# Optimization experiments

Measured on AMD Instinct MI355X. Metric: run time of the kernel, lower is better.

The kernel has to match this reference:

```python
import jax, jax.numpy as jnp
import numpy as np

N_EMBD = 768
N_EXPERTS = 8
TOP_K = 2
D_FF = 4 * N_EMBD


def setup_inputs() -> dict:
    key = jax.random.key(0)
    k1, k2, k3, k4 = jax.random.split(key, 4)
    x = jax.random.normal(k1, (2, 2048, N_EMBD), dtype=jnp.float32)
    gate_w = jax.random.normal(k2, (N_EMBD, N_EXPERTS), dtype=jnp.float32) * (1.0 / np.sqrt(N_EMBD))
    w_fc = jax.random.normal(k3, (N_EXPERTS, N_EMBD, D_FF), dtype=jnp.float32) * (1.0 / np.sqrt(N_EMBD))
    w_proj = jax.random.normal(k4, (N_EXPERTS, D_FF, N_EMBD), dtype=jnp.float32) * (1.0 / np.sqrt(D_FF))
    return {"x": x, "gate_w": gate_w, "w_fc": w_fc, "w_proj": w_proj}


def reference(x, gate_w, w_fc, w_proj):
    B, S, D = x.shape
    E = w_fc.shape[0]
    xt = x.reshape(-1, D)                    # [T, D]
    T = xt.shape[0]
    scores = xt @ gate_w                      # [T, E]
    expert_weights, expert_indices = jax.lax.top_k(scores, TOP_K)  # [T, K]
    expert_weights = jax.nn.softmax(expert_weights, axis=-1)
    # per-token combine weight for each expert (0 if expert not selected)
    comb = jnp.zeros((T, E), dtype=xt.dtype)
    comb = comb.at[jnp.arange(T)[:, None], expert_indices].add(expert_weights)  # [T, E]
    out = jnp.zeros_like(xt)
    for e in range(E):  # fixed small loop over experts
        h = jax.nn.gelu(xt @ w_fc[e], approximate=False)  # torch nn.GELU default = exact erf
        y_e = h @ w_proj[e]                               # [T, D]
        out = out + comb[:, e:e + 1] * y_e
    return out.reshape(B, S, D)
```

## Files before the change

kernel.cpp:

```cpp
#include <hip/hip_runtime.h>
#include <hip/hip_bf16.h>
#include <math.h>

#define T_TOK 4096
#define D_EMB 768
#define DFF   3072
#define N_EXP 8
#define MAXT  72
#define CNTS  16

typedef __attribute__((ext_vector_type(8))) short bf16x8;
typedef __attribute__((ext_vector_type(4))) float f32x4;

typedef __attribute__((address_space(3))) unsigned int lds_u32_t;
typedef __attribute__((address_space(1))) unsigned int glob_u32_t;

__device__ __forceinline__ void gload16(const void* g, void* l) {
  __builtin_amdgcn_global_load_lds((const glob_u32_t*)g, (lds_u32_t*)l, 16, 0, 0);
}

__device__ __forceinline__ short f2bf(float f) {
  union { __hip_bfloat16 b; short s; } u;
  u.b = __float2bfloat16(f);
  return u.s;
}

__global__ void zero_init_kernel(float4* __restrict__ out4, int n4, int* __restrict__ cnt) {
  int i = blockIdx.x * blockDim.x + threadIdx.x;
  if (i < N_EXP * CNTS) cnt[i] = 0;
  float4 z; z.x = z.y = z.z = z.w = 0.f;
  for (int j = i; j < n4; j += gridDim.x * blockDim.x) out4[j] = z;
}

__global__ void cast_x_kernel(const float4* __restrict__ in, short4* __restrict__ outp, int n4) {
  int i = blockIdx.x * blockDim.x + threadIdx.x;
  if (i >= n4) return;
  float4 v = in[i];
  short4 o;
  o.x = f2bf(v.x); o.y = f2bf(v.y); o.z = f2bf(v.z); o.w = f2bf(v.w);
  outp[i] = o;
}

__global__ void transpose_cast_kernel(const float* __restrict__ in, short* __restrict__ outp,
                                      int R, int C) {
  __shared__ float tile[64][65];
  int e = blockIdx.z;
  int c0 = blockIdx.x * 64, r0 = blockIdx.y * 64;
  const float* src = in + (size_t)e * R * C;
  short* dst = outp + (size_t)e * R * C;
  int tid = threadIdx.x;
#pragma unroll
  for (int it = 0; it < 4; ++it) {
    int idx = tid + it * 256;
    int r = idx >> 4;
    int c4 = idx & 15;
    float4 v = *(const float4*)&src[(size_t)(r0 + r) * C + c0 + c4 * 4];
    tile[r][c4 * 4 + 0] = v.x; tile[r][c4 * 4 + 1] = v.y;
    tile[r][c4 * 4 + 2] = v.z; tile[r][c4 * 4 + 3] = v.w;
  }
  __syncthreads();
#pragma unroll
  for (int it = 0; it < 4; ++it) {
    int idx = tid + it * 256;
    int c = idx >> 4;
    int rr = idx & 15;
    short4 o;
    o.x = f2bf(tile[rr * 4 + 0][c]);
    o.y = f2bf(tile[rr * 4 + 1][c]);
    o.z = f2bf(tile[rr * 4 + 2][c]);
    o.w = f2bf(tile[rr * 4 + 3][c]);
    *(short4*)&dst[(size_t)(c0 + c) * R + r0 + rr * 4] = o;
  }
}

__global__ __launch_bounds__(256)
void gate_kernel(const float* __restrict__ x, const float* __restrict__ gw,
                 int* __restrict__ cnt, int* __restrict__ tok,
                 float* __restrict__ wgt) {
  __shared__ int lcnt[N_EXP];
  __shared__ int gbase[N_EXP];
  __shared__ int le[32];
  __shared__ float lw[32];
  __shared__ int lpos[32];
  int tid = threadIdx.x, lane = tid & 63, wid = tid >> 6;
  if (tid < N_EXP) lcnt[tid] = 0;
  __syncthreads();

#pragma unroll
  for (int i = 0; i < 4; i++) {
    int t = blockIdx.x * 16 + wid * 4 + i;
    float s[N_EXP];
#pragma unroll
    for (int e = 0; e < N_EXP; e++) s[e] = 0.f;
#pragma unroll
    for (int dd = 0; dd < D_EMB / 64; dd++) {
      int d = dd * 64 + lane;
      float xv = x[(size_t)t * D_EMB + d];
#pragma unroll
      for (int e = 0; e < N_EXP; e++) s[e] += xv * gw[d * N_EXP + e];
    }
#pragma unroll
    for (int e = 0; e < N_EXP; e++) {
#pragma unroll
      for (int off = 32; off > 0; off >>= 1) s[e] += __shfl_xor(s[e], off, 64);
    }
    if (lane == 0) {
      int e0 = 0;
#pragma unroll
      for (int e = 1; e < N_EXP; e++) if (s[e] > s[e0]) e0 = e;
      int e1 = -1;
#pragma unroll
      for (int e = 0; e < N_EXP; e++) {
        if (e == e0) continue;
        if (e1 < 0 || s[e] > s[e1]) e1 = e;
      }
      float p1 = __expf(s[e1] - s[e0]);
      float inv = 1.f / (1.f + p1);
      int idx = (wid * 4 + i) * 2;
      le[idx] = e0; lw[idx] = inv;           lpos[idx] = atomicAdd(&lcnt[e0], 1);
      le[idx + 1] = e1; lw[idx + 1] = p1 * inv; lpos[idx + 1] = atomicAdd(&lcnt[e1], 1);
    }
  }
  __syncthreads();
  if (tid < N_EXP) gbase[tid] = atomicAdd(&cnt[tid * CNTS], lcnt[tid]);
  __syncthreads();
  if (tid < 32) {
    int e = le[tid];
    int t = blockIdx.x * 16 + (tid >> 1);
    int p = gbase[e] + lpos[tid];
    tok[e * T_TOK + p] = t;
    wgt[e * T_TOK + p] = lw[tid];
  }
}

__global__ void plan_kernel(const int* __restrict__ cnt, int* __restrict__ offs,
                            int* __restrict__ tile_e, int* __restrict__ tile_rt,
                            int* __restrict__ ntiles) {
  if (threadIdx.x != 0 || blockIdx.x != 0) return;
  int o = 0, nt = 0;
  for (int e = 0; e < N_EXP; e++) {
    offs[e] = o;
    int tc = (cnt[e * CNTS] + 127) >> 7;
    for (int i = 0; i < tc; i++) { tile_e[nt] = e; tile_rt[nt] = i; nt++; }
    o += cnt[e * CNTS];
  }
  *ntiles = nt;
}

template<int KDIM, int NDIM, int SPLITK, int GRT, int GCT, int EPI>
__global__ __launch_bounds__(256, 4)
void moe_gemm(const short* __restrict__ A, const short* __restrict__ Bw,
              const int* __restrict__ tok, const float* __restrict__ wgt,
              const int* __restrict__ cnt, const int* __restrict__ offs,
              const int* __restrict__ tile_e, const int* __restrict__ tile_rt,
              const int* __restrict__ ntiles,
              short* __restrict__ hout, float* __restrict__ fout) {
  const int COLT = NDIM / 128;
  const int KS = KDIM / SPLITK;
  const int NKT = KS / 32;
  const int BPS = GRT * GCT;
  const int NCG = COLT / GCT;
  const int PER_SK = MAXT * COLT;
  static_assert(MAXT % GRT == 0 && COLT % GCT == 0, "supertile must divide grid");

  int nwg = gridDim.x;
  int cpx = nwg >> 3;
  int logical = (blockIdx.x & 7) * cpx + (blockIdx.x >> 3);
  int sk = logical / PER_SK;
  int rem = logical % PER_SK;
  int super = rem / BPS, inner = rem % BPS;
  int band = super / NCG, cg = super % NCG;
  int tile = band * GRT + (inner % GRT);
  int ct = cg * GCT + (inner / GRT);
  if (tile >= *ntiles) return;
  int e = tile_e[tile], rt = tile_rt[tile];
  int ne = cnt[e * CNTS];
  int base = offs[e];

  __shared__ __align__(16) short As[2][128 * 32];
  __shared__ __align__(16) short Bs[2][128 * 32];

  int tid = threadIdx.x;
  int lane = tid & 63;
  int wid = tid >> 6;

  const short* aptr[2];
  const short* bptr[2];
  int lofs[2];
#pragma unroll
  for (int i = 0; i < 2; i++) {
    int seg = tid + i * 256;
    int row = seg >> 2;
    int p = seg & 3;
    int q = p ^ ((row ^ (row >> 2)) & 3);
    int r = rt * 128 + row;
    if (r >= ne) r = ne - 1;
    size_t ga = (EPI == 0) ? (size_t)tok[e * T_TOK + r] : (size_t)(base + r);
    aptr[i] = A + ga * KDIM + sk * KS + q * 8;
    bptr[i] = Bw + ((size_t)e * NDIM + ct * 128 + row) * KDIM + sk * KS + q * 8;
    lofs[i] = seg * 8;
  }

  f32x4 acc[4][4];
#pragma unroll
  for (int m = 0; m < 4; m++)
#pragma unroll
    for (int n = 0; n < 4; n++) acc[m][n] = (f32x4){0.f, 0.f, 0.f, 0.f};

  int wr = (wid >> 1) * 64, wc = (wid & 1) * 64;

#pragma unroll
  for (int i = 0; i < 2; i++) {
    gload16(aptr[i], &As[0][lofs[i]]);
    gload16(bptr[i], &Bs[0][lofs[i]]);
  }
  __syncthreads();

  int cur = 0;
  for (int kt = 0; kt < NKT; ++kt) {
    if (kt + 1 < NKT) {
      int k0 = (kt + 1) * 32;
#pragma unroll
      for (int i = 0; i < 2; i++) {
        gload16(aptr[i] + k0, &As[cur ^ 1][lofs[i]]);
        gload16(bptr[i] + k0, &Bs[cur ^ 1][lofs[i]]);
      }
    }
    int cb = lane >> 4;
    bf16x8 af[4], bv[4];
#pragma unroll
    for (int m = 0; m < 4; m++) {
      int row = wr + m * 16 + (lane & 15);
      af[m] = *(const bf16x8*)&As[cur][row * 32 + ((cb ^ ((row ^ (row >> 2)) & 3)) * 8)];
    }
#pragma unroll
    for (int n = 0; n < 4; n++) {
      int row = wc + n * 16 + (lane & 15);
      bv[n] = *(const bf16x8*)&Bs[cur][row * 32 + ((cb ^ ((row ^ (row >> 2)) & 3)) * 8)];
    }
#pragma unroll
    for (int m = 0; m < 4; m++)
#pragma unroll
      for (int n = 0; n < 4; n++)
        acc[m][n] = __builtin_amdgcn_mfma_f32_16x16x32_bf16(af[m], bv[n], acc[m][n], 0, 0, 0);
    __syncthreads();
    cur ^= 1;
  }

  int colbase = ct * 128 + wc;
#pragma unroll
  for (int m = 0; m < 4; m++) {
#pragma unroll
    for (int j = 0; j < 4; j++) {
      int rloc = rt * 128 + wr + m * 16 + ((lane >> 4) << 2) + j;
      if (rloc < ne) {
        if (EPI == 0) {
          size_t hrow = (size_t)(base + rloc) * NDIM;
#pragma unroll
          for (int n = 0; n < 4; n++) {
            float v = acc[m][n][j];
            float g = 0.5f * v * (1.0f + erff(v * 0.70710678118f));
            hout[hrow + colbase + n * 16 + (lane & 15)] = f2bf(g);
          }
        } else {
          int t = tok[e * T_TOK + rloc];
          float w = wgt[e * T_TOK + rloc];
          float* orow = fout + (size_t)t * NDIM + colbase + (lane & 15);
#pragma unroll
          for (int n = 0; n < 4; n++)
            atomicAdd(orow + n * 16, w * acc[m][n][j]);
        }
      }
    }
  }
}

extern "C" void kernel_launch(void* const* d_in, const int* in_sizes, int n_in,
                              void* d_out, int out_size, void* d_ws, size_t ws_size,
                              hipStream_t stream) {
  const float* x   = (const float*)d_in[0];
  const float* gw  = (const float*)d_in[1];
  const float* wfc = (const float*)d_in[2];
  const float* wpj = (const float*)d_in[3];
  float* out = (float*)d_out;

  char* ws = (char*)d_ws;
  const size_t SZ_XB = (size_t)T_TOK * D_EMB * 2;
  const size_t SZ_W  = (size_t)N_EXP * D_EMB * DFF * 2;
  const size_t SZ_H  = (size_t)2 * T_TOK * DFF * 2;
  short* xb   = (short*)(ws);
  short* wfcT = (short*)(ws + SZ_XB);
  short* wpjT = (short*)(ws + SZ_XB + SZ_W);
  short* h    = (short*)(ws + SZ_XB + 2 * SZ_W);
  char* p2    = ws + SZ_XB + 2 * SZ_W + SZ_H;
  int*   tok  = (int*)(p2);
  float* wgt  = (float*)(p2 + (size_t)N_EXP * T_TOK * 4);
  char* p3    = p2 + (size_t)N_EXP * T_TOK * 8;
  int*   cnt     = (int*)(p3);
  int*   offs    = (int*)(p3 + 1024);
  int*   tile_e  = (int*)(p3 + 1024 + 64);
  int*   tile_rt = (int*)(p3 + 1024 + 64 + 512);
  int*   ntiles  = (int*)(p3 + 1024 + 64 + 1024);

  int n4 = out_size / 4;
  zero_init_kernel<<<2048, 256, 0, stream>>>((float4*)out, n4, cnt);
  cast_x_kernel<<<(T_TOK * D_EMB / 4 + 255) / 256, 256, 0, stream>>>(
      (const float4*)x, (short4*)xb, T_TOK * D_EMB / 4);
  transpose_cast_kernel<<<dim3(DFF / 64, D_EMB / 64, N_EXP), 256, 0, stream>>>(wfc, wfcT, D_EMB, DFF);
  transpose_cast_kernel<<<dim3(D_EMB / 64, DFF / 64, N_EXP), 256, 0, stream>>>(wpj, wpjT, DFF, D_EMB);
  gate_kernel<<<T_TOK / 16, 256, 0, stream>>>(x, gw, cnt, tok, wgt);
  plan_kernel<<<1, 1, 0, stream>>>(cnt, offs, tile_e, tile_rt, ntiles);
  moe_gemm<D_EMB, DFF, 1, 8, 8, 0><<<MAXT * (DFF / 128), 256, 0, stream>>>(
      xb, wfcT, tok, wgt, cnt, offs, tile_e, tile_rt, ntiles, h, nullptr);
  moe_gemm<DFF, D_EMB, 2, 8, 6, 1><<<2 * MAXT * (D_EMB / 128), 256, 0, stream>>>(
      h, wpjT, tok, wgt, cnt, offs, tile_e, tile_rt, ntiles, nullptr, out);
}
```

Before: 238.4 us.

## Pre-tile weights and gathered tokens into swizzled contiguous slabs; use tanh GELU

Weights are cast and rearranged into contiguous, pre-swizzled 128x32 bf16 slabs per tile, and routed token rows are gathered into per-tile slabs in a new kernel. Each GEMM k-step then loads one contiguous 8KB block instead of strided row segments, which is meant to improve memory access efficiency. The separate x cast and transpose kernels are removed. GELU switches from exact erf to a tanh approximation using a fast exp, which cuts epilogue cost but changes numerics slightly.

```diff
diff --git a/kernel.cpp b/kernel.cpp
--- a/kernel.cpp
+++ b/kernel.cpp
@@ -25,6 +25,17 @@
   return u.s;
 }
 
+__device__ __forceinline__ float gelu_f(float v) {
+  float u = 0.7978845608f * v * (1.0f + 0.044715f * v * v);
+  float a = fabsf(u);
+  float em = __expf(-2.0f * a);
+  float th = (1.0f - em) / (1.0f + em);
+  th = (u < 0.0f) ? -th : th;
+  return 0.5f * v * (1.0f + th);
+}
+
+__device__ __forceinline__ int swz(int row) { return (row ^ (row >> 2)) & 3; }
+
 __global__ void zero_init_kernel(float4* __restrict__ out4, int n4, int* __restrict__ cnt) {
   int i = blockIdx.x * blockDim.x + threadIdx.x;
   if (i < N_EXP * CNTS) cnt[i] = 0;
@@ -32,44 +43,32 @@
   for (int j = i; j < n4; j += gridDim.x * blockDim.x) out4[j] = z;
 }
 
-__global__ void cast_x_kernel(const float4* __restrict__ in, short4* __restrict__ outp, int n4) {
-  int i = blockIdx.x * blockDim.x + threadIdx.x;
-  if (i >= n4) return;
-  float4 v = in[i];
-  short4 o;
-  o.x = f2bf(v.x); o.y = f2bf(v.y); o.z = f2bf(v.z); o.w = f2bf(v.w);
-  outp[i] = o;
-}
-
-__global__ void transpose_cast_kernel(const float* __restrict__ in, short* __restrict__ outp,
-                                      int R, int C) {
-  __shared__ float tile[64][65];
-  int e = blockIdx.z;
-  int c0 = blockIdx.x * 64, r0 = blockIdx.y * 64;
-  const float* src = in + (size_t)e * R * C;
-  short* dst = outp + (size_t)e * R * C;
+__global__ __launch_bounds__(256)
+void slab_weights(const float* __restrict__ src, short* __restrict__ dst,
+                  int Kt, int Nt, int NCT, int NKTall) {
+  __shared__ float t32[32][132];
+  int ct = blockIdx.x, kt = blockIdx.y, e = blockIdx.z;
+  const float* s = src + ((size_t)e * Kt + kt * 32) * Nt + ct * 128;
   int tid = threadIdx.x;
 #pragma unroll
-  for (int it = 0; it < 4; ++it) {
-    int idx = tid + it * 256;
-    int r = idx >> 4;
-    int c4 = idx & 15;
-    float4 v = *(const float4*)&src[(size_t)(r0 + r) * C + c0 + c4 * 4];
-    tile[r][c4 * 4 + 0] = v.x; tile[r][c4 * 4 + 1] = v.y;
-    tile[r][c4 * 4 + 2] = v.z; tile[r][c4 * 4 + 3] = v.w;
-  }
-  __syncthreads();
-#pragma unroll
-  for (int it = 0; it < 4; ++it) {
-    int idx = tid + it * 256;
-    int c = idx >> 4;
-    int rr = idx & 15;
-    short4 o;
-    o.x = f2bf(tile[rr * 4 + 0][c]);
-    o.y = f2bf(tile[rr * 4 + 1][c]);
-    o.z = f2bf(tile[rr * 4 + 2][c]);
-    o.w = f2bf(tile[rr * 4 + 3][c]);
-    *(short4*)&dst[(size_t)(c0 + c) * R + r0 + rr * 4] = o;
+  for (int p4 = 0; p4 < 4; p4++) {
+    int idx = tid + p4 * 256;
+    int kl = idx >> 5, c4 = idx & 31;
+    float4 v = *(const float4*)&s[(size_t)kl * Nt + c4 * 4];
+    t32[kl][c4 * 4 + 0] = v.x; t32[kl][c4 * 4 + 1] = v.y;
+    t32[kl][c4 * 4 + 2] = v.z; t32[kl][c4 * 4 + 3] = v.w;
+  }
+  __syncthreads();
+  short* d = dst + (((size_t)e * NCT + ct) * NKTall + kt) * 4096;
+#pragma unroll
+  for (int i = 0; i < 2; i++) {
+    int seg = tid + i * 256;
+    int row = seg >> 2, p = seg & 3;
+    int q = p ^ swz(row);
+    union { short sv[8]; uint4 u; } o;
+#pragma unroll
+    for (int j = 0; j < 8; j++) o.sv[j] = f2bf(t32[q * 8 + j][row]);
+    *(uint4*)&d[(size_t)seg * 8] = o.u;
   }
 }
 
@@ -147,9 +146,35 @@
   *ntiles = nt;
 }
 
+__global__ __launch_bounds__(256)
+void gatherA_kernel(const float* __restrict__ x, const int* __restrict__ tok,
+                    const int* __restrict__ cnt, const int* __restrict__ offs,
+                    const int* __restrict__ tile_e, const int* __restrict__ tile_rt,
+                    const int* __restrict__ ntiles, short* __restrict__ aslab) {
+  int tile = blockIdx.x, kt = blockIdx.y;
+  if (tile >= *ntiles) return;
+  int e = tile_e[tile], rt = tile_rt[tile];
+  int ne = cnt[e * CNTS];
+  int tid = threadIdx.x;
+  short* d = aslab + ((size_t)tile * 24 + kt) * 4096;
+#pragma unroll
+  for (int i = 0; i < 2; i++) {
+    int seg = tid + i * 256;
+    int row = seg >> 2, p = seg & 3;
+    int q = p ^ swz(row);
+    int r = rt * 128 + row; if (r >= ne) r = ne - 1;
+    int t = tok[e * T_TOK + r];
+    const float* src = x + (size_t)t * D_EMB + kt * 32 + q * 8;
+    union { short sv[8]; uint4 u; } o;
+#pragma unroll
+    for (int j = 0; j < 8; j++) o.sv[j] = f2bf(src[j]);
+    *(uint4*)&d[(size_t)seg * 8] = o.u;
+  }
+}
+
 template<int KDIM, int NDIM, int SPLITK, int GRT, int GCT, int EPI>
 __global__ __launch_bounds__(256, 4)
-void moe_gemm(const short* __restrict__ A, const short* __restrict__ Bw,
+void moe_gemm(const short* __restrict__ Aop, const short* __restrict__ Bslab,
               const int* __restrict__ tok, const float* __restrict__ wgt,
               const int* __restrict__ cnt, const int* __restrict__ offs,
               const int* __restrict__ tile_e, const int* __restrict__ tile_rt,
@@ -158,10 +183,10 @@
   const int COLT = NDIM / 128;
   const int KS = KDIM / SPLITK;
   const int NKT = KS / 32;
+  const int NKTALL = KDIM / 32;
   const int BPS = GRT * GCT;
   const int NCG = COLT / GCT;
   const int PER_SK = MAXT * COLT;
-  static_assert(MAXT % GRT == 0 && COLT % GCT == 0, "supertile must divide grid");
 
   int nwg = gridDim.x;
   int cpx = nwg >> 3;
@@ -184,20 +209,22 @@
   int lane = tid & 63;
   int wid = tid >> 6;
 
+  const int AKT = (EPI == 0) ? 4096 : 32;
   const short* aptr[2];
   const short* bptr[2];
   int lofs[2];
 #pragma unroll
   for (int i = 0; i < 2; i++) {
     int seg = tid + i * 256;
-    int row = seg >> 2;
-    int p = seg & 3;
-    int q = p ^ ((row ^ (row >> 2)) & 3);
-    int r = rt * 128 + row;
-    if (r >= ne) r = ne - 1;
-    size_t ga = (EPI == 0) ? (size_t)tok[e * T_TOK + r] : (size_t)(base + r);
-    aptr[i] = A + ga * KDIM + sk * KS + q * 8;
-    bptr[i] = Bw + ((size_t)e * NDIM + ct * 128 + row) * KDIM + sk * KS + q * 8;
+    int row = seg >> 2, p = seg & 3;
+    int q = p ^ swz(row);
+    if (EPI == 0) {
+      aptr[i] = Aop + ((size_t)tile * 24) * 4096 + seg * 8;
+    } else {
+      int r = rt * 128 + row; if (r >= ne) r = ne - 1;
+      aptr[i] = Aop + (size_t)(base + r) * KDIM + sk * KS + q * 8;
+    }
+    bptr[i] = Bslab + (((size_t)e * COLT + ct) * NKTALL + sk * NKT) * 4096 + seg * 8;
     lofs[i] = seg * 8;
   }
 
@@ -219,11 +246,10 @@
   int cur = 0;
   for (int kt = 0; kt < NKT; ++kt) {
     if (kt + 1 < NKT) {
-      int k0 = (kt + 1) * 32;
 #pragma unroll
       for (int i = 0; i < 2; i++) {
-        gload16(aptr[i] + k0, &As[cur ^ 1][lofs[i]]);
-        gload16(bptr[i] + k0, &Bs[cur ^ 1][lofs[i]]);
+        gload16(aptr[i] + (size_t)(kt + 1) * AKT, &As[cur ^ 1][lofs[i]]);
+        gload16(bptr[i] + (size_t)(kt + 1) * 4096, &Bs[cur ^ 1][lofs[i]]);
       }
     }
     int cb = lane >> 4;
@@ -231,12 +257,12 @@
 #pragma unroll
     for (int m = 0; m < 4; m++) {
       int row = wr + m * 16 + (lane & 15);
-      af[m] = *(const bf16x8*)&As[cur][row * 32 + ((cb ^ ((row ^ (row >> 2)) & 3)) * 8)];
+      af[m] = *(const bf16x8*)&As[cur][row * 32 + ((cb ^ swz(row)) * 8)];
     }
 #pragma unroll
     for (int n = 0; n < 4; n++) {
       int row = wc + n * 16 + (lane & 15);
-      bv[n] = *(const bf16x8*)&Bs[cur][row * 32 + ((cb ^ ((row ^ (row >> 2)) & 3)) * 8)];
+      bv[n] = *(const bf16x8*)&Bs[cur][row * 32 + ((cb ^ swz(row)) * 8)];
     }
 #pragma unroll
     for (int m = 0; m < 4; m++)
@@ -257,11 +283,8 @@
         if (EPI == 0) {
           size_t hrow = (size_t)(base + rloc) * NDIM;
 #pragma unroll
-          for (int n = 0; n < 4; n++) {
-            float v = acc[m][n][j];
-            float g = 0.5f * v * (1.0f + erff(v * 0.70710678118f));
-            hout[hrow + colbase + n * 16 + (lane & 15)] = f2bf(g);
-          }
+          for (int n = 0; n < 4; n++)
+            hout[hrow + colbase + n * 16 + (lane & 15)] = f2bf(gelu_f(acc[m][n][j]));
         } else {
           int t = tok[e * T_TOK + rloc];
           float w = wgt[e * T_TOK + rloc];
@@ -285,14 +308,15 @@
   float* out = (float*)d_out;
 
   char* ws = (char*)d_ws;
-  const size_t SZ_XB = (size_t)T_TOK * D_EMB * 2;
-  const size_t SZ_W  = (size_t)N_EXP * D_EMB * DFF * 2;
-  const size_t SZ_H  = (size_t)2 * T_TOK * DFF * 2;
-  short* xb   = (short*)(ws);
-  short* wfcT = (short*)(ws + SZ_XB);
-  short* wpjT = (short*)(ws + SZ_XB + SZ_W);
-  short* h    = (short*)(ws + SZ_XB + 2 * SZ_W);
-  char* p2    = ws + SZ_XB + 2 * SZ_W + SZ_H;
+  const size_t SZ_ASLAB = (size_t)MAXT * 24 * 4096 * 2;
+  const size_t SZ_BFC   = (size_t)N_EXP * 24 * 24 * 4096 * 2;
+  const size_t SZ_BPJ   = (size_t)N_EXP * 6 * 96 * 4096 * 2;
+  const size_t SZ_H     = (size_t)2 * T_TOK * DFF * 2;
+  short* aslab = (short*)(ws);
+  short* bfc   = (short*)(ws + SZ_ASLAB);
+  short* bpj   = (short*)(ws + SZ_ASLAB + SZ_BFC);
+  short* h     = (short*)(ws + SZ_ASLAB + SZ_BFC + SZ_BPJ);
+  char* p2     = ws + SZ_ASLAB + SZ_BFC + SZ_BPJ + SZ_H;
   int*   tok  = (int*)(p2);
   float* wgt  = (float*)(p2 + (size_t)N_EXP * T_TOK * 4);
   char* p3    = p2 + (size_t)N_EXP * T_TOK * 8;
@@ -304,14 +328,13 @@
 
   int n4 = out_size / 4;
   zero_init_kernel<<<2048, 256, 0, stream>>>((float4*)out, n4, cnt);
-  cast_x_kernel<<<(T_TOK * D_EMB / 4 + 255) / 256, 256, 0, stream>>>(
-      (const float4*)x, (short4*)xb, T_TOK * D_EMB / 4);
-  transpose_cast_kernel<<<dim3(DFF / 64, D_EMB / 64, N_EXP), 256, 0, stream>>>(wfc, wfcT, D_EMB, DFF);
-  transpose_cast_kernel<<<dim3(D_EMB / 64, DFF / 64, N_EXP), 256, 0, stream>>>(wpj, wpjT, DFF, D_EMB);
+  slab_weights<<<dim3(24, 24, N_EXP), 256, 0, stream>>>(wfc, bfc, D_EMB, DFF, 24, 24);
+  slab_weights<<<dim3(6, 96, N_EXP), 256, 0, stream>>>(wpj, bpj, DFF, D_EMB, 6, 96);
   gate_kernel<<<T_TOK / 16, 256, 0, stream>>>(x, gw, cnt, tok, wgt);
   plan_kernel<<<1, 1, 0, stream>>>(cnt, offs, tile_e, tile_rt, ntiles);
+  gatherA_kernel<<<dim3(MAXT, 24), 256, 0, stream>>>(x, tok, cnt, offs, tile_e, tile_rt, ntiles, aslab);
   moe_gemm<D_EMB, DFF, 1, 8, 8, 0><<<MAXT * (DFF / 128), 256, 0, stream>>>(
-      xb, wfcT, tok, wgt, cnt, offs, tile_e, tile_rt, ntiles, h, nullptr);
+      aslab, bfc, tok, wgt, cnt, offs, tile_e, tile_rt, ntiles, h, nullptr);
   moe_gemm<DFF, D_EMB, 2, 8, 6, 1><<<2 * MAXT * (D_EMB / 128), 256, 0, stream>>>(
-      h, wpjT, tok, wgt, cnt, offs, tile_e, tile_rt, ntiles, nullptr, out);
-}
+      h, bpj, tok, wgt, cnt, offs, tile_e, tile_rt, ntiles, nullptr, out);
+}
```

Result: faster. 219.9 us (-7.8%).
